# Kernel optimization log

Hardware: AMD Instinct MI355X
Metric: run time of the kernel (lower is better)

## Reference

```python
import jax, jax.numpy as jnp
import numpy as np

HEADS = 4
HID = 128
NEG_SLOPE = 0.2
N_NODES = 20000
N_EDGES = 320000
N_GRAPHS = 64
IN_DIM = 12


def gat_layer(x, src, dst, W, a_src, a_dst, b, n):
    # PyG GATConv, heads=4, concat=False (mean over heads), add_self_loops handled by caller.
    h = (x @ W).reshape(n, HEADS, HID)                      # [N,H,C]
    e_src = jnp.einsum('nhc,hc->nh', h, a_src)              # [N,H]
    e_dst = jnp.einsum('nhc,hc->nh', h, a_dst)
    e = jax.nn.leaky_relu(e_src[src] + e_dst[dst], NEG_SLOPE)  # [E,H]
    m = jax.lax.stop_gradient(jax.ops.segment_max(e, dst, num_segments=n))
    ex = jnp.exp(e - m[dst])
    denom = jax.ops.segment_sum(ex, dst, num_segments=n)    # [N,H]
    alpha = ex / denom[dst]                                 # edge softmax over incoming edges
    out = jax.ops.segment_sum(alpha[:, :, None] * h[src], dst, num_segments=n)  # [N,H,C]
    return out.mean(axis=1) + b                             # concat=False -> head mean, then bias


def setup_inputs() -> dict:
    key = jax.random.key(0)
    ks = jax.random.split(key, 20)
    def glorot(k, shape):
        lim = float(np.sqrt(6.0 / (shape[0] + shape[-1])))
        return jax.random.uniform(k, shape, jnp.float32, -lim, lim)
    inp = {
        'x': jax.random.normal(ks[0], (N_NODES, IN_DIM), jnp.float32),
        'edge_index': jax.random.randint(ks[1], (2, N_EDGES), 0, N_NODES, jnp.int64 if jax.config.jax_enable_x64 else jnp.int32),
        'batch': jnp.sort(jax.random.randint(ks[2], (N_NODES,), 0, N_GRAPHS)),
        'batch_size_tensor': jax.random.uniform(ks[3], (N_GRAPHS, 1), jnp.float32),
        # GAT layer 1
        'W1': glorot(ks[4], (IN_DIM, HEADS * HID)), 'as1': glorot(ks[5], (HEADS, HID)),
        'ad1': glorot(ks[6], (HEADS, HID)), 'b1': jnp.zeros((HID,), jnp.float32),
        # GAT layer 2
        'W2': glorot(ks[7], (HID, HEADS * HID)), 'as2': glorot(ks[8], (HEADS, HID)),
        'ad2': glorot(ks[9], (HEADS, HID)), 'b2': jnp.zeros((HID,), jnp.float32),
        # GAT layer 3
        'W3': glorot(ks[10], (HID, HEADS * HID)), 'as3': glorot(ks[11], (HEADS, HID)),
        'ad3': glorot(ks[12], (HEADS, HID)), 'b3': jnp.zeros((HID,), jnp.float32),
        # MLP: (128+1)->128->64->2
        'M1': glorot(ks[13], (HID + 1, HID)), 'mb1': jnp.zeros((HID,), jnp.float32),
        'M2': glorot(ks[14], (HID, HID // 2)), 'mb2': jnp.zeros((HID // 2,), jnp.float32),
        'M3': glorot(ks[15], (HID // 2, 2)), 'mb3': jnp.zeros((2,), jnp.float32),
    }
    return inp


def reference(x, edge_index, batch, batch_size_tensor,
              W1, as1, ad1, b1, W2, as2, ad2, b2, W3, as3, ad3, b3,
              M1, mb1, M2, mb2, M3, mb3):
    n = x.shape[0]
    loops = jnp.arange(n, dtype=edge_index.dtype)
    src = jnp.concatenate([edge_index[0], loops])   # add_self_loops=True (PyG default)
    dst = jnp.concatenate([edge_index[1], loops])
    h = jax.nn.relu(gat_layer(x, src, dst, W1, as1, ad1, b1, n))
    h = jax.nn.relu(gat_layer(h, src, dst, W2, as2, ad2, b2, n))
    h = jax.nn.relu(gat_layer(h, src, dst, W3, as3, ad3, b3, n))
    # global mean pool over graphs
    g = batch_size_tensor.shape[0]
    sums = jax.ops.segment_sum(h, batch, num_segments=g)
    cnts = jax.ops.segment_sum(jnp.ones((n,), h.dtype), batch, num_segments=g)
    pooled = sums / jnp.maximum(cnts, 1.0)[:, None]          # [G,128]
    bs = jnp.log1p(batch_size_tensor)                        # [G,1]
    z = jnp.concatenate([pooled, bs], axis=1)                # [G,129]
    z = jax.nn.relu(z @ M1 + mb1)                            # dropout(0.2) is identity at eval
    z = jax.nn.relu(z @ M2 + mb2)
    return z @ M3 + mb3                                      # [G,2]
```

## Files before the change

### kernel.cpp

```cpp
#include <hip/hip_runtime.h>
#include <hip/hip_bf16.h>
#include <math.h>

#define NN 20000
#define NE 320000
#define ET (NE + NN)
#define NG 64
#define HEADS 4
#define HID 128
#define OUTC (HEADS * HID)
#define SLOPE 0.2f

__device__ __forceinline__ float lrelu(float v) { return v > 0.f ? v : SLOPE * v; }

__global__ void k_hist(const int* __restrict__ ei, int* __restrict__ deg) {
  int e = blockIdx.x * blockDim.x + threadIdx.x;
  if (e >= ET) return;
  int dst = (e < NE) ? ei[NE + e] : (e - NE);
  atomicAdd(&deg[dst], 1);
}

__global__ void k_scan(const int* __restrict__ deg, int* __restrict__ row_start,
                       int* __restrict__ cursor) {
  __shared__ int sums[1024];
  int tid = threadIdx.x;
  const int PER = (NN + 1023) / 1024;
  int base = tid * PER;
  int local = 0;
  for (int i = 0; i < PER; ++i) { int idx = base + i; if (idx < NN) local += deg[idx]; }
  sums[tid] = local;
  __syncthreads();
  for (int off = 1; off < 1024; off <<= 1) {
    int v = (tid >= off) ? sums[tid - off] : 0;
    __syncthreads();
    sums[tid] += v;
    __syncthreads();
  }
  int run = sums[tid] - local;
  for (int i = 0; i < PER; ++i) {
    int idx = base + i;
    if (idx < NN) { row_start[idx] = run; cursor[idx] = run; run += deg[idx]; }
  }
  if (tid == 1023) row_start[NN] = sums[1023];
}

__global__ void k_scatter(const int* __restrict__ ei, int* __restrict__ cursor,
                          int* __restrict__ csr_src) {
  int e = blockIdx.x * blockDim.x + threadIdx.x;
  if (e >= ET) return;
  int src, dst;
  if (e < NE) { src = ei[e]; dst = ei[NE + e]; }
  else        { src = e - NE; dst = src; }
  int pos = atomicAdd(&cursor[dst], 1);
  csr_src[pos] = src;
}

__global__ void k_watt3(const float* __restrict__ W1, const float* __restrict__ as1,
                        const float* __restrict__ ad1, const float* __restrict__ W2,
                        const float* __restrict__ as2, const float* __restrict__ ad2,
                        const float* __restrict__ W3, const float* __restrict__ as3,
                        const float* __restrict__ ad3, float* __restrict__ watt1,
                        float* __restrict__ watt2, float* __restrict__ watt3) {
  int b = blockIdx.x;
  const float *W, *as, *ad;
  float* wo;
  int k;
  if (b < 12)       { k = b;       W = W1; as = as1; ad = ad1; wo = watt1; }
  else if (b < 140) { k = b - 12;  W = W2; as = as2; ad = ad2; wo = watt2; }
  else              { k = b - 140; W = W3; as = as3; ad = ad3; wo = watt3; }
  int tid = threadIdx.x;
  int t = tid & 7, h = t & 3;
  int c0 = (tid >> 3) * 4;
  const float* av = (t < 4 ? as : ad) + h * HID;
  const float* wr = W + (size_t)k * OUTC + h * HID;
  float4 wv = *reinterpret_cast<const float4*>(&wr[c0]);
  float4 a4 = *reinterpret_cast<const float4*>(&av[c0]);
  float p = wv.x * a4.x + wv.y * a4.y + wv.z * a4.z + wv.w * a4.w;
  __shared__ float lp[32][8];
  lp[tid >> 3][t] = p;
  __syncthreads();
  if (tid < 8) {
    float s = 0.f;
    for (int cc = 0; cc < 32; ++cc) s += lp[cc][tid];
    wo[k * 8 + tid] = s;
  }
}

__global__ void k_esd1(const float* __restrict__ x, const float* __restrict__ watt,
                       float* __restrict__ es, float* __restrict__ ed) {
  int n = blockIdx.x * blockDim.x + threadIdx.x;
  if (n >= NN) return;
  float xr[12];
#pragma unroll
  for (int k = 0; k < 12; ++k) xr[k] = x[(size_t)n * 12 + k];
#pragma unroll
  for (int t = 0; t < 8; ++t) {
    float acc = 0.f;
#pragma unroll
    for (int k = 0; k < 12; ++k) acc += xr[k] * watt[k * 8 + t];
    if (t < 4) es[n * 4 + t] = acc;
    else       ed[n * 4 + (t - 4)] = acc;
  }
}

__global__ void __launch_bounds__(256) k_esd128(
    const float* __restrict__ x, const float* __restrict__ watt,
    float* __restrict__ es, float* __restrict__ ed) {
  __shared__ float sw[HID * 8];
  int tid = threadIdx.x;
  for (int i = tid; i < HID * 8; i += 256) sw[i] = watt[i];
  __syncthreads();
  int wid = tid >> 6, lane = tid & 63;
  int gw = blockIdx.x * 4 + wid;
  int nw = gridDim.x * 4;
  for (int n = gw; n < NN; n += nw) {
    float2 xv = *reinterpret_cast<const float2*>(&x[(size_t)n * HID + lane * 2]);
    float p[8];
#pragma unroll
    for (int t = 0; t < 8; ++t)
      p[t] = xv.x * sw[(lane * 2) * 8 + t] + xv.y * sw[(lane * 2 + 1) * 8 + t];
#pragma unroll
    for (int t = 0; t < 8; ++t) {
#pragma unroll
      for (int off = 1; off < 64; off <<= 1) p[t] += __shfl_xor(p[t], off);
    }
    if (lane == 0) {
      es[n * 4 + 0] = p[0]; es[n * 4 + 1] = p[1];
      es[n * 4 + 2] = p[2]; es[n * 4 + 3] = p[3];
      ed[n * 4 + 0] = p[4]; ed[n * 4 + 1] = p[5];
      ed[n * 4 + 2] = p[6]; ed[n * 4 + 3] = p[7];
    }
  }
}

__global__ void __launch_bounds__(256) k_prep(
    const float* __restrict__ es, const float* __restrict__ ed,
    const int* __restrict__ row_start, const int* __restrict__ csr_src,
    float* __restrict__ ealpha, float* __restrict__ invd) {
  int wid = threadIdx.x >> 6;
  int lane = threadIdx.x & 63;
  int n = blockIdx.x * 4 + wid;
  int start = row_start[n];
  int deg = row_start[n + 1] - start;
  float4 edv = *reinterpret_cast<const float4*>(&ed[(size_t)n * 4]);
  float d0 = 0.f, d1 = 0.f, d2 = 0.f, d3 = 0.f;
  for (int k = lane; k < deg; k += 64) {
    int s = csr_src[start + k];
    float4 e4 = *reinterpret_cast<const float4*>(&es[(size_t)s * 4]);
    float4 ex;
    ex.x = __expf(lrelu(e4.x + edv.x));
    ex.y = __expf(lrelu(e4.y + edv.y));
    ex.z = __expf(lrelu(e4.z + edv.z));
    ex.w = __expf(lrelu(e4.w + edv.w));
    *reinterpret_cast<float4*>(&ealpha[(size_t)(start + k) * 4]) = ex;
    d0 += ex.x; d1 += ex.y; d2 += ex.z; d3 += ex.w;
  }
#pragma unroll
  for (int off = 1; off < 64; off <<= 1) {
    d0 += __shfl_xor(d0, off);
    d1 += __shfl_xor(d1, off);
    d2 += __shfl_xor(d2, off);
    d3 += __shfl_xor(d3, off);
  }
  if (lane == 0) {
    float4 iv;
    iv.x = 0.25f / d0; iv.y = 0.25f / d1; iv.z = 0.25f / d2; iv.w = 0.25f / d3;
    *reinterpret_cast<float4*>(&invd[(size_t)n * 4]) = iv;
  }
}

__global__ void __launch_bounds__(256, 4) k_aggx128(
    const float* __restrict__ x, const float* __restrict__ ealpha,
    const float* __restrict__ invd, const int* __restrict__ row_start,
    const int* __restrict__ csr_src, float* __restrict__ z) {
  int wid = threadIdx.x >> 6;
  int lane = threadIdx.x & 63;
  int n = blockIdx.x * 4 + wid;
  int start = row_start[n];
  int deg = row_start[n + 1] - start;
  const int* sp = csr_src + start;
  const float4* ap4 = reinterpret_cast<const float4*>(ealpha) + start;
  int c = lane * 2;
  float2 a0c = make_float2(0.f, 0.f), a1c = make_float2(0.f, 0.f);
  float2 a2c = make_float2(0.f, 0.f), a3c = make_float2(0.f, 0.f);
  int j = 0;
  for (; j + 4 <= deg; j += 4) {
    int s0 = sp[j + 0], s1 = sp[j + 1], s2 = sp[j + 2], s3 = sp[j + 3];
    float4 q0 = ap4[j + 0], q1 = ap4[j + 1], q2 = ap4[j + 2], q3 = ap4[j + 3];
    float2 x0 = *reinterpret_cast<const float2*>(&x[(size_t)s0 * HID + c]);
    float2 x1 = *reinterpret_cast<const float2*>(&x[(size_t)s1 * HID + c]);
    float2 x2 = *reinterpret_cast<const float2*>(&x[(size_t)s2 * HID + c]);
    float2 x3 = *reinterpret_cast<const float2*>(&x[(size_t)s3 * HID + c]);
    a0c.x += q0.x * x0.x; a0c.y += q0.x * x0.y;
    a1c.x += q0.y * x0.x; a1c.y += q0.y * x0.y;
    a2c.x += q0.z * x0.x; a2c.y += q0.z * x0.y;
    a3c.x += q0.w * x0.x; a3c.y += q0.w * x0.y;
    a0c.x += q1.x * x1.x; a0c.y += q1.x * x1.y;
    a1c.x += q1.y * x1.x; a1c.y += q1.y * x1.y;
    a2c.x += q1.z * x1.x; a2c.y += q1.z * x1.y;
    a3c.x += q1.w * x1.x; a3c.y += q1.w * x1.y;
    a0c.x += q2.x * x2.x; a0c.y += q2.x * x2.y;
    a1c.x += q2.y * x2.x; a1c.y += q2.y * x2.y;
    a2c.x += q2.z * x2.x; a2c.y += q2.z * x2.y;
    a3c.x += q2.w * x2.x; a3c.y += q2.w * x2.y;
    a0c.x += q3.x * x3.x; a0c.y += q3.x * x3.y;
    a1c.x += q3.y * x3.x; a1c.y += q3.y * x3.y;
    a2c.x += q3.z * x3.x; a2c.y += q3.z * x3.y;
    a3c.x += q3.w * x3.x; a3c.y += q3.w * x3.y;
  }
  for (; j < deg; ++j) {
    int s = sp[j];
    float4 q = ap4[j];
    float2 xv = *reinterpret_cast<const float2*>(&x[(size_t)s * HID + c]);
    a0c.x += q.x * xv.x; a0c.y += q.x * xv.y;
    a1c.x += q.y * xv.x; a1c.y += q.y * xv.y;
    a2c.x += q.z * xv.x; a2c.y += q.z * xv.y;
    a3c.x += q.w * xv.x; a3c.y += q.w * xv.y;
  }
  float4 iv = *reinterpret_cast<const float4*>(&invd[(size_t)n * 4]);
  a0c.x *= iv.x; a0c.y *= iv.x;
  a1c.x *= iv.y; a1c.y *= iv.y;
  a2c.x *= iv.z; a2c.y *= iv.z;
  a3c.x *= iv.w; a3c.y *= iv.w;
  float* zr = z + (size_t)n * OUTC;
  *reinterpret_cast<float2*>(&zr[0 * HID + c]) = a0c;
  *reinterpret_cast<float2*>(&zr[1 * HID + c]) = a1c;
  *reinterpret_cast<float2*>(&zr[2 * HID + c]) = a2c;
  *reinterpret_cast<float2*>(&zr[3 * HID + c]) = a3c;
}

__global__ void __launch_bounds__(256, 4) k_aggx1(
    const float* __restrict__ x, const float* __restrict__ ealpha,
    const float* __restrict__ invd, const int* __restrict__ row_start,
    const int* __restrict__ csr_src, float* __restrict__ z1) {
  int wid = threadIdx.x >> 6;
  int lane = threadIdx.x & 63;
  int n = blockIdx.x * 4 + wid;
  int start = row_start[n];
  int deg = row_start[n + 1] - start;
  const int* sp = csr_src + start;
  const float4* ap4 = reinterpret_cast<const float4*>(ealpha) + start;
  int h = lane >> 4;
  int cr = lane & 15;
  int cc = cr < 12 ? cr : 11;
  float acc = 0.f;
  int j = 0;
  for (; j + 4 <= deg; j += 4) {
    int s0 = sp[j + 0], s1 = sp[j + 1], s2 = sp[j + 2], s3 = sp[j + 3];
    float4 q0 = ap4[j + 0], q1 = ap4[j + 1], q2 = ap4[j + 2], q3 = ap4[j + 3];
    float ah0 = (h == 0) ? q0.x : (h == 1) ? q0.y : (h == 2) ? q0.z : q0.w;
    float ah1 = (h == 0) ? q1.x : (h == 1) ? q1.y : (h == 2) ? q1.z : q1.w;
    float ah2 = (h == 0) ? q2.x : (h == 1) ? q2.y : (h == 2) ? q2.z : q2.w;
    float ah3 = (h == 0) ? q3.x : (h == 1) ? q3.y : (h == 2) ? q3.z : q3.w;
    float x0 = x[(size_t)s0 * 12 + cc];
    float x1 = x[(size_t)s1 * 12 + cc];
    float x2 = x[(size_t)s2 * 12 + cc];
    float x3 = x[(size_t)s3 * 12 + cc];
    acc += ah0 * x0 + ah1 * x1 + ah2 * x2 + ah3 * x3;
  }
  for (; j < deg; ++j) {
    int s = sp[j];
    float4 q = ap4[j];
    float ah = (h == 0) ? q.x : (h == 1) ? q.y : (h == 2) ? q.z : q.w;
    acc += ah * x[(size_t)s * 12 + cc];
  }
  float ivh = invd[(size_t)n * 4 + h];
  if (cr < 12) z1[(size_t)n * 48 + h * 12 + cr] = acc * ivh;
}

template <int KTOT, int KH, int BK>
__global__ void k_gemm_full(const float* __restrict__ z, const float* __restrict__ W,
                            const float* __restrict__ bias, float* __restrict__ xout) {
  const int BM = 64, BN = 64;
  __shared__ float sAT[BK][BM + 4];
  __shared__ float sB[BK][BN];
  int tid = threadIdx.x;
  int r0 = blockIdx.y * BM;
  int cb = blockIdx.x * BN;
  int tx = tid & 15, ty = tid >> 4;
  int m0 = ty * 4, n0 = tx * 4;
  float acc[4][4] = {};
  for (int k0 = 0; k0 < KTOT; k0 += BK) {
    const int AF4 = BM * BK / 4;
    for (int idx = tid; idx < AF4; idx += 256) {
      int r = idx / (BK / 4);
      int kq = idx % (BK / 4);
      int row = r0 + r;
      float4 v = make_float4(0.f, 0.f, 0.f, 0.f);
      if (row < NN) v = *reinterpret_cast<const float4*>(&z[(size_t)row * KTOT + k0 + kq * 4]);
      sAT[kq * 4 + 0][r] = v.x;
      sAT[kq * 4 + 1][r] = v.y;
      sAT[kq * 4 + 2][r] = v.z;
      sAT[kq * 4 + 3][r] = v.w;
    }
    const int BF4 = BK * BN / 4;
    for (int idx = tid; idx < BF4; idx += 256) {
      int kr = idx / 16, nq = idx & 15;
      int kk = k0 + kr;
      int h = kk / KH, k = kk % KH;
      float4 v = *reinterpret_cast<const float4*>(&W[(size_t)k * OUTC + h * HID + cb + nq * 4]);
      *reinterpret_cast<float4*>(&sB[kr][nq * 4]) = v;
    }
    __syncthreads();
#pragma unroll 4
    for (int kk = 0; kk < BK; ++kk) {
      float4 a = *reinterpret_cast<const float4*>(&sAT[kk][m0]);
      float4 b = *reinterpret_cast<const float4*>(&sB[kk][n0]);
      acc[0][0] += a.x * b.x; acc[0][1] += a.x * b.y; acc[0][2] += a.x * b.z; acc[0][3] += a.x * b.w;
      acc[1][0] += a.y * b.x; acc[1][1] += a.y * b.y; acc[1][2] += a.y * b.z; acc[1][3] += a.y * b.w;
      acc[2][0] += a.z * b.x; acc[2][1] += a.z * b.y; acc[2][2] += a.z * b.z; acc[2][3] += a.z * b.w;
      acc[3][0] += a.w * b.x; acc[3][1] += a.w * b.y; acc[3][2] += a.w * b.z; acc[3][3] += a.w * b.w;
    }
    __syncthreads();
  }
  float4 bv = *reinterpret_cast<const float4*>(&bias[cb + n0]);
#pragma unroll
  for (int i = 0; i < 4; ++i) {
    int row = r0 + m0 + i;
    if (row < NN) {
      float4 o;
      o.x = fmaxf(acc[i][0] + bv.x, 0.f);
      o.y = fmaxf(acc[i][1] + bv.y, 0.f);
      o.z = fmaxf(acc[i][2] + bv.z, 0.f);
      o.w = fmaxf(acc[i][3] + bv.w, 0.f);
      *reinterpret_cast<float4*>(&xout[(size_t)row * HID + cb + n0]) = o;
    }
  }
}

template <int KTOT, int KH, int BK, int KCH>
__global__ void k_gemm_ks(const float* __restrict__ z, const float* __restrict__ W,
                          float* __restrict__ part) {
  const int BM = 64, BN = 64;
  __shared__ float sAT[BK][BM + 4];
  __shared__ float sB[BK][BN];
  int tid = threadIdx.x;
  int r0 = blockIdx.y * BM;
  int cb = blockIdx.x * BN;
  int kc = blockIdx.z;
  int tx = tid & 15, ty = tid >> 4;
  int m0 = ty * 4, n0 = tx * 4;
  float acc[4][4] = {};
  for (int k0 = kc * KCH; k0 < (kc + 1) * KCH; k0 += BK) {
    const int AF4 = BM * BK / 4;
    for (int idx = tid; idx < AF4; idx += 256) {
      int r = idx / (BK / 4);
      int kq = idx % (BK / 4);
      int row = r0 + r;
      float4 v = make_float4(0.f, 0.f, 0.f, 0.f);
      if (row < NN) v = *reinterpret_cast<const float4*>(&z[(size_t)row * KTOT + k0 + kq * 4]);
      sAT[kq * 4 + 0][r] = v.x;
      sAT[kq * 4 + 1][r] = v.y;
      sAT[kq * 4 + 2][r] = v.z;
      sAT[kq * 4 + 3][r] = v.w;
    }
    const int BF4 = BK * BN / 4;
    for (int idx = tid; idx < BF4; idx += 256) {
      int kr = idx / 16, nq = idx & 15;
      int kk = k0 + kr;
      int h = kk / KH, k = kk % KH;
      float4 v = *reinterpret_cast<const float4*>(&W[(size_t)k * OUTC + h * HID + cb + nq * 4]);
      *reinterpret_cast<float4*>(&sB[kr][nq * 4]) = v;
    }
    __syncthreads();
#pragma unroll 4
    for (int kk = 0; kk < BK; ++kk) {
      float4 a = *reinterpret_cast<const float4*>(&sAT[kk][m0]);
      float4 b = *reinterpret_cast<const float4*>(&sB[kk][n0]);
      acc[0][0] += a.x * b.x; acc[0][1] += a.x * b.y; acc[0][2] += a.x * b.z; acc[0][3] += a.x * b.w;
      acc[1][0] += a.y * b.x; acc[1][1] += a.y * b.y; acc[1][2] += a.y * b.z; acc[1][3] += a.y * b.w;
      acc[2][0] += a.z * b.x; acc[2][1] += a.z * b.y; acc[2][2] += a.z * b.z; acc[2][3] += a.z * b.w;
      acc[3][0] += a.w * b.x; acc[3][1] += a.w * b.y; acc[3][2] += a.w * b.z; acc[3][3] += a.w * b.w;
    }
    __syncthreads();
  }
#pragma unroll
  for (int i = 0; i < 4; ++i) {
    int row = r0 + m0 + i;
    if (row < NN) {
      float4 v = make_float4(acc[i][0], acc[i][1], acc[i][2], acc[i][3]);
      *reinterpret_cast<float4*>(&part[((size_t)kc * NN + row) * HID + cb + n0]) = v;
    }
  }
}

template <int POOL, int NKC>
__global__ void k_epi(const float* __restrict__ part, const float* __restrict__ bias,
                      const int* __restrict__ batch, float* __restrict__ xout,
                      float* __restrict__ gsums) {
  int tid = threadIdx.x;
  int row = blockIdx.x * 2 + (tid >> 7);
  int c = tid & 127;
  float o = bias[c];
#pragma unroll
  for (int kc = 0; kc < NKC; ++kc)
    o += part[((size_t)kc * NN + row) * HID + c];
  o = fmaxf(o, 0.f);
  if (POOL) {
    atomicAdd(&gsums[(size_t)batch[row] * HID + c], o);
  } else {
    xout[(size_t)row * HID + c] = o;
  }
}

__global__ void k_mlp(const float* __restrict__ sums, const int* __restrict__ batch,
                      const float* __restrict__ bst, const float* __restrict__ M1,
                      const float* __restrict__ mb1, const float* __restrict__ M2,
                      const float* __restrict__ mb2, const float* __restrict__ M3,
                      const float* __restrict__ mb3, float* __restrict__ out) {
  int g = blockIdx.x, tid = threadIdx.x;
  int lo = 0, hi = NN;
  while (lo < hi) { int mid = (lo + hi) >> 1; if (batch[mid] < g) lo = mid + 1; else hi = mid; }
  int s = lo;
  lo = s; hi = NN;
  while (lo < hi) { int mid = (lo + hi) >> 1; if (batch[mid] < g + 1) lo = mid + 1; else hi = mid; }
  int e = lo;
  float cnt = (float)(e - s);
  float pooled = sums[g * HID + tid] / fmaxf(cnt, 1.f);
  __shared__ float z[HID + 1];
  __shared__ float z1[HID];
  __shared__ float z2[64];
  z[tid] = pooled;
  if (tid == 0) z[HID] = log1pf(bst[g]);
  __syncthreads();
  float a1 = mb1[tid];
  for (int k = 0; k < HID + 1; ++k) a1 += z[k] * M1[k * HID + tid];
  z1[tid] = a1 > 0.f ? a1 : 0.f;
  __syncthreads();
  if (tid < 64) {
    float a2 = mb2[tid];
    for (int k = 0; k < HID; ++k) a2 += z1[k] * M2[k * 64 + tid];
    z2[tid] = a2 > 0.f ? a2 : 0.f;
  }
  __syncthreads();
  if (tid < 2) {
    float a3 = mb3[tid];
    for (int k = 0; k < 64; ++k) a3 += z2[k] * M3[k * 2 + tid];
    out[g * 2 + tid] = a3;
  }
}

extern "C" void kernel_launch(void* const* d_in, const int* in_sizes, int n_in,
                              void* d_out, int out_size, void* d_ws, size_t ws_size,
                              hipStream_t stream) {
  const float* x   = (const float*)d_in[0];
  const int*   ei  = (const int*)d_in[1];
  const int*   bat = (const int*)d_in[2];
  const float* bst = (const float*)d_in[3];
  const float* W1 = (const float*)d_in[4];
  const float* as1 = (const float*)d_in[5];
  const float* ad1 = (const float*)d_in[6];
  const float* b1 = (const float*)d_in[7];
  const float* W2 = (const float*)d_in[8];
  const float* as2 = (const float*)d_in[9];
  const float* ad2 = (const float*)d_in[10];
  const float* b2 = (const float*)d_in[11];
  const float* W3 = (const float*)d_in[12];
  const float* as3 = (const float*)d_in[13];
  const float* ad3 = (const float*)d_in[14];
  const float* b3 = (const float*)d_in[15];
  const float* M1 = (const float*)d_in[16];
  const float* mb1 = (const float*)d_in[17];
  const float* M2 = (const float*)d_in[18];
  const float* mb2 = (const float*)d_in[19];
  const float* M3 = (const float*)d_in[20];
  const float* mb3 = (const float*)d_in[21];
  float* out = (float*)d_out;

  const bool use4 = ws_size >= (size_t)110 * 1024 * 1024;

  char* ws = (char*)d_ws;
  auto alloc = [&](size_t bytes) -> void* {
    void* p = (void*)ws;
    ws += (bytes + 255) & ~(size_t)255;
    return p;
  };
  float* z_buf  = (float*)alloc((size_t)NN * OUTC * 4);
  float* z1_buf = (float*)alloc((size_t)NN * 48 * 4);
  float* x_buf  = (float*)alloc((size_t)NN * HID * 4);
  float* e_src  = (float*)alloc((size_t)NN * 4 * 4);
  float* e_dst  = (float*)alloc((size_t)NN * 4 * 4);
  int*   deg    = (int*)alloc((size_t)NN * 4);
  int*   rowst  = (int*)alloc((size_t)(NN + 1) * 4);
  int*   cursor = (int*)alloc((size_t)NN * 4);
  int*   csr    = (int*)alloc((size_t)ET * 4);
  float* ealpha = (float*)alloc((size_t)ET * 4 * 4);
  float* part   = (float*)alloc((size_t)(use4 ? 4 : 2) * NN * HID * 4);
  float* invd   = (float*)alloc((size_t)NN * 4 * 4);
  float* watt1  = (float*)alloc((size_t)12 * 8 * 4);
  float* watt2  = (float*)alloc((size_t)HID * 8 * 4);
  float* watt3  = (float*)alloc((size_t)HID * 8 * 4);
  float* gsums  = (float*)alloc((size_t)NG * HID * 4);

  hipMemsetAsync(deg, 0, (size_t)NN * 4, stream);
  hipMemsetAsync(gsums, 0, (size_t)NG * HID * 4, stream);
  k_hist<<<(ET + 255) / 256, 256, 0, stream>>>(ei, deg);
  k_scan<<<1, 1024, 0, stream>>>(deg, rowst, cursor);
  k_scatter<<<(ET + 255) / 256, 256, 0, stream>>>(ei, cursor, csr);
  k_watt3<<<268, 256, 0, stream>>>(W1, as1, ad1, W2, as2, ad2, W3, as3, ad3,
                                   watt1, watt2, watt3);

  dim3 pgrid(NN / 4);
  dim3 g1grid(2, (NN + 63) / 64);
  dim3 ks4grid(2, (NN + 63) / 64, 4);
  dim3 ks2grid(2, (NN + 63) / 64, 2);
  dim3 epigrid(NN / 2);
  k_esd1<<<(NN + 255) / 256, 256, 0, stream>>>(x, watt1, e_src, e_dst);
  k_prep<<<pgrid, 256, 0, stream>>>(e_src, e_dst, rowst, csr, ealpha, invd);
  k_aggx1<<<pgrid, 256, 0, stream>>>(x, ealpha, invd, rowst, csr, z1_buf);
  k_gemm_full<48, 12, 48><<<g1grid, 256, 0, stream>>>(z1_buf, W1, b1, x_buf);
  k_esd128<<<512, 256, 0, stream>>>(x_buf, watt2, e_src, e_dst);
  k_prep<<<pgrid, 256, 0, stream>>>(e_src, e_dst, rowst, csr, ealpha, invd);
  k_aggx128<<<pgrid, 256, 0, stream>>>(x_buf, ealpha, invd, rowst, csr, z_buf);
  if (use4) {
    k_gemm_ks<512, 128, 64, 128><<<ks4grid, 256, 0, stream>>>(z_buf, W2, part);
    k_epi<0, 4><<<epigrid, 256, 0, stream>>>(part, b2, bat, x_buf, gsums);
  } else {
    k_gemm_ks<512, 128, 64, 256><<<ks2grid, 256, 0, stream>>>(z_buf, W2, part);
    k_epi<0, 2><<<epigrid, 256, 0, stream>>>(part, b2, bat, x_buf, gsums);
  }
  k_esd128<<<512, 256, 0, stream>>>(x_buf, watt3, e_src, e_dst);
  k_prep<<<pgrid, 256, 0, stream>>>(e_src, e_dst, rowst, csr, ealpha, invd);
  k_aggx128<<<pgrid, 256, 0, stream>>>(x_buf, ealpha, invd, rowst, csr, z_buf);
  if (use4) {
    k_gemm_ks<512, 128, 64, 128><<<ks4grid, 256, 0, stream>>>(z_buf, W3, part);
    k_epi<1, 4><<<epigrid, 256, 0, stream>>>(part, b3, bat, x_buf, gsums);
  } else {
    k_gemm_ks<512, 128, 64, 256><<<ks2grid, 256, 0, stream>>>(z_buf, W3, part);
    k_epi<1, 2><<<epigrid, 256, 0, stream>>>(part, b3, bat, x_buf, gsums);
  }
  k_mlp<<<NG, 128, 0, stream>>>(gsums, bat, bst, M1, mb1, M2, mb2, M3, mb3, out);
}
```

Before: 378.9 us.

## Fuse edge-softmax prep into aggregation kernels via per-wave LDS staging

```diff
diff --git a/kernel.cpp b/kernel.cpp
--- a/kernel.cpp
+++ b/kernel.cpp
@@ -133,95 +133,90 @@
   }
 }
 
-__global__ void __launch_bounds__(256) k_prep(
-    const float* __restrict__ es, const float* __restrict__ ed,
-    const int* __restrict__ row_start, const int* __restrict__ csr_src,
-    float* __restrict__ ealpha, float* __restrict__ invd) {
-  int wid = threadIdx.x >> 6;
-  int lane = threadIdx.x & 63;
-  int n = blockIdx.x * 4 + wid;
-  int start = row_start[n];
-  int deg = row_start[n + 1] - start;
-  float4 edv = *reinterpret_cast<const float4*>(&ed[(size_t)n * 4]);
-  float d0 = 0.f, d1 = 0.f, d2 = 0.f, d3 = 0.f;
-  for (int k = lane; k < deg; k += 64) {
-    int s = csr_src[start + k];
-    float4 e4 = *reinterpret_cast<const float4*>(&es[(size_t)s * 4]);
-    float4 ex;
-    ex.x = __expf(lrelu(e4.x + edv.x));
-    ex.y = __expf(lrelu(e4.y + edv.y));
-    ex.z = __expf(lrelu(e4.z + edv.z));
-    ex.w = __expf(lrelu(e4.w + edv.w));
-    *reinterpret_cast<float4*>(&ealpha[(size_t)(start + k) * 4]) = ex;
-    d0 += ex.x; d1 += ex.y; d2 += ex.z; d3 += ex.w;
-  }
-#pragma unroll
-  for (int off = 1; off < 64; off <<= 1) {
-    d0 += __shfl_xor(d0, off);
-    d1 += __shfl_xor(d1, off);
-    d2 += __shfl_xor(d2, off);
-    d3 += __shfl_xor(d3, off);
-  }
-  if (lane == 0) {
-    float4 iv;
-    iv.x = 0.25f / d0; iv.y = 0.25f / d1; iv.z = 0.25f / d2; iv.w = 0.25f / d3;
-    *reinterpret_cast<float4*>(&invd[(size_t)n * 4]) = iv;
-  }
-}
-
-__global__ void __launch_bounds__(256, 4) k_aggx128(
-    const float* __restrict__ x, const float* __restrict__ ealpha,
-    const float* __restrict__ invd, const int* __restrict__ row_start,
+__global__ void __launch_bounds__(256, 4) k_aggf(
+    const float* __restrict__ x, const float* __restrict__ es,
+    const float* __restrict__ ed, const int* __restrict__ row_start,
     const int* __restrict__ csr_src, float* __restrict__ z) {
+  __shared__ float sal[4][256];
   int wid = threadIdx.x >> 6;
   int lane = threadIdx.x & 63;
   int n = blockIdx.x * 4 + wid;
   int start = row_start[n];
   int deg = row_start[n + 1] - start;
   const int* sp = csr_src + start;
-  const float4* ap4 = reinterpret_cast<const float4*>(ealpha) + start;
+  float4 edv = *reinterpret_cast<const float4*>(&ed[(size_t)n * 4]);
   int c = lane * 2;
   float2 a0c = make_float2(0.f, 0.f), a1c = make_float2(0.f, 0.f);
   float2 a2c = make_float2(0.f, 0.f), a3c = make_float2(0.f, 0.f);
-  int j = 0;
-  for (; j + 4 <= deg; j += 4) {
-    int s0 = sp[j + 0], s1 = sp[j + 1], s2 = sp[j + 2], s3 = sp[j + 3];
-    float4 q0 = ap4[j + 0], q1 = ap4[j + 1], q2 = ap4[j + 2], q3 = ap4[j + 3];
-    float2 x0 = *reinterpret_cast<const float2*>(&x[(size_t)s0 * HID + c]);
-    float2 x1 = *reinterpret_cast<const float2*>(&x[(size_t)s1 * HID + c]);
-    float2 x2 = *reinterpret_cast<const float2*>(&x[(size_t)s2 * HID + c]);
-    float2 x3 = *reinterpret_cast<const float2*>(&x[(size_t)s3 * HID + c]);
-    a0c.x += q0.x * x0.x; a0c.y += q0.x * x0.y;
-    a1c.x += q0.y * x0.x; a1c.y += q0.y * x0.y;
-    a2c.x += q0.z * x0.x; a2c.y += q0.z * x0.y;
-    a3c.x += q0.w * x0.x; a3c.y += q0.w * x0.y;
-    a0c.x += q1.x * x1.x; a0c.y += q1.x * x1.y;
-    a1c.x += q1.y * x1.x; a1c.y += q1.y * x1.y;
-    a2c.x += q1.z * x1.x; a2c.y += q1.z * x1.y;
-    a3c.x += q1.w * x1.x; a3c.y += q1.w * x1.y;
-    a0c.x += q2.x * x2.x; a0c.y += q2.x * x2.y;
-    a1c.x += q2.y * x2.x; a1c.y += q2.y * x2.y;
-    a2c.x += q2.z * x2.x; a2c.y += q2.z * x2.y;
-    a3c.x += q2.w * x2.x; a3c.y += q2.w * x2.y;
-    a0c.x += q3.x * x3.x; a0c.y += q3.x * x3.y;
-    a1c.x += q3.y * x3.x; a1c.y += q3.y * x3.y;
-    a2c.x += q3.z * x3.x; a2c.y += q3.z * x3.y;
-    a3c.x += q3.w * x3.x; a3c.y += q3.w * x3.y;
-  }
-  for (; j < deg; ++j) {
-    int s = sp[j];
-    float4 q = ap4[j];
-    float2 xv = *reinterpret_cast<const float2*>(&x[(size_t)s * HID + c]);
-    a0c.x += q.x * xv.x; a0c.y += q.x * xv.y;
-    a1c.x += q.y * xv.x; a1c.y += q.y * xv.y;
-    a2c.x += q.z * xv.x; a2c.y += q.z * xv.y;
-    a3c.x += q.w * xv.x; a3c.y += q.w * xv.y;
-  }
-  float4 iv = *reinterpret_cast<const float4*>(&invd[(size_t)n * 4]);
-  a0c.x *= iv.x; a0c.y *= iv.x;
-  a1c.x *= iv.y; a1c.y *= iv.y;
-  a2c.x *= iv.z; a2c.y *= iv.z;
-  a3c.x *= iv.w; a3c.y *= iv.w;
+  float d0 = 0.f, d1 = 0.f, d2 = 0.f, d3 = 0.f;
+  for (int cb = 0; cb < deg; cb += 64) {
+    int m = min(64, deg - cb);
+    {
+      int kk = cb + ((lane < m) ? lane : (m - 1));
+      int s = sp[kk];
+      float4 e4 = *reinterpret_cast<const float4*>(&es[(size_t)s * 4]);
+      float4 ex;
+      ex.x = __expf(lrelu(e4.x + edv.x));
+      ex.y = __expf(lrelu(e4.y + edv.y));
+      ex.z = __expf(lrelu(e4.z + edv.z));
+      ex.w = __expf(lrelu(e4.w + edv.w));
+      if (lane < m) {
+        *reinterpret_cast<float4*>(&sal[wid][lane * 4]) = ex;
+        d0 += ex.x; d1 += ex.y; d2 += ex.z; d3 += ex.w;
+      }
+    }
+    asm volatile("s_waitcnt lgkmcnt(0)" ::: "memory");
+    int j = 0;
+    for (; j + 4 <= m; j += 4) {
+      float4 q0 = *reinterpret_cast<const float4*>(&sal[wid][(j + 0) * 4]);
+      float4 q1 = *reinterpret_cast<const float4*>(&sal[wid][(j + 1) * 4]);
+      float4 q2 = *reinterpret_cast<const float4*>(&sal[wid][(j + 2) * 4]);
+      float4 q3 = *reinterpret_cast<const float4*>(&sal[wid][(j + 3) * 4]);
+      int s0 = sp[cb + j + 0], s1 = sp[cb + j + 1];
+      int s2 = sp[cb + j + 2], s3 = sp[cb + j + 3];
+      float2 x0 = *reinterpret_cast<const float2*>(&x[(size_t)s0 * HID + c]);
+      float2 x1 = *reinterpret_cast<const float2*>(&x[(size_t)s1 * HID + c]);
+      float2 x2 = *reinterpret_cast<const float2*>(&x[(size_t)s2 * HID + c]);
+      float2 x3 = *reinterpret_cast<const float2*>(&x[(size_t)s3 * HID + c]);
+      a0c.x += q0.x * x0.x; a0c.y += q0.x * x0.y;
+      a1c.x += q0.y * x0.x; a1c.y += q0.y * x0.y;
+      a2c.x += q0.z * x0.x; a2c.y += q0.z * x0.y;
+      a3c.x += q0.w * x0.x; a3c.y += q0.w * x0.y;
+      a0c.x += q1.x * x1.x; a0c.y += q1.x * x1.y;
+      a1c.x += q1.y * x1.x; a1c.y += q1.y * x1.y;
+      a2c.x += q1.z * x1.x; a2c.y += q1.z * x1.y;
+      a3c.x += q1.w * x1.x; a3c.y += q1.w * x1.y;
+      a0c.x += q2.x * x2.x; a0c.y += q2.x * x2.y;
+      a1c.x += q2.y * x2.x; a1c.y += q2.y * x2.y;
+      a2c.x += q2.z * x2.x; a2c.y += q2.z * x2.y;
+      a3c.x += q2.w * x2.x; a3c.y += q2.w * x2.y;
+      a0c.x += q3.x * x3.x; a0c.y += q3.x * x3.y;
+      a1c.x += q3.y * x3.x; a1c.y += q3.y * x3.y;
+      a2c.x += q3.z * x3.x; a2c.y += q3.z * x3.y;
+      a3c.x += q3.w * x3.x; a3c.y += q3.w * x3.y;
+    }
+    for (; j < m; ++j) {
+      float4 q = *reinterpret_cast<const float4*>(&sal[wid][j * 4]);
+      int s = sp[cb + j];
+      float2 xv = *reinterpret_cast<const float2*>(&x[(size_t)s * HID + c]);
+      a0c.x += q.x * xv.x; a0c.y += q.x * xv.y;
+      a1c.x += q.y * xv.x; a1c.y += q.y * xv.y;
+      a2c.x += q.z * xv.x; a2c.y += q.z * xv.y;
+      a3c.x += q.w * xv.x; a3c.y += q.w * xv.y;
+    }
+  }
+#pragma unroll
+  for (int off = 1; off < 64; off <<= 1) {
+    d0 += __shfl_xor(d0, off);
+    d1 += __shfl_xor(d1, off);
+    d2 += __shfl_xor(d2, off);
+    d3 += __shfl_xor(d3, off);
+  }
+  float i0 = 0.25f / d0, i1 = 0.25f / d1, i2 = 0.25f / d2, i3 = 0.25f / d3;
+  a0c.x *= i0; a0c.y *= i0;
+  a1c.x *= i1; a1c.y *= i1;
+  a2c.x *= i2; a2c.y *= i2;
+  a3c.x *= i3; a3c.y *= i3;
   float* zr = z + (size_t)n * OUTC;
   *reinterpret_cast<float2*>(&zr[0 * HID + c]) = a0c;
   *reinterpret_cast<float2*>(&zr[1 * HID + c]) = a1c;
@@ -229,42 +224,69 @@
   *reinterpret_cast<float2*>(&zr[3 * HID + c]) = a3c;
 }
 
-__global__ void __launch_bounds__(256, 4) k_aggx1(
-    const float* __restrict__ x, const float* __restrict__ ealpha,
-    const float* __restrict__ invd, const int* __restrict__ row_start,
+__global__ void __launch_bounds__(256, 4) k_aggf1(
+    const float* __restrict__ x, const float* __restrict__ es,
+    const float* __restrict__ ed, const int* __restrict__ row_start,
     const int* __restrict__ csr_src, float* __restrict__ z1) {
+  __shared__ float sal[4][256];
   int wid = threadIdx.x >> 6;
   int lane = threadIdx.x & 63;
   int n = blockIdx.x * 4 + wid;
   int start = row_start[n];
   int deg = row_start[n + 1] - start;
   const int* sp = csr_src + start;
-  const float4* ap4 = reinterpret_cast<const float4*>(ealpha) + start;
+  float4 edv = *reinterpret_cast<const float4*>(&ed[(size_t)n * 4]);
   int h = lane >> 4;
   int cr = lane & 15;
   int cc = cr < 12 ? cr : 11;
   float acc = 0.f;
-  int j = 0;
-  for (; j + 4 <= deg; j += 4) {
-    int s0 = sp[j + 0], s1 = sp[j + 1], s2 = sp[j + 2], s3 = sp[j + 3];
-    float4 q0 = ap4[j + 0], q1 = ap4[j + 1], q2 = ap4[j + 2], q3 = ap4[j + 3];
-    float ah0 = (h == 0) ? q0.x : (h == 1) ? q0.y : (h == 2) ? q0.z : q0.w;
-    float ah1 = (h == 0) ? q1.x : (h == 1) ? q1.y : (h == 2) ? q1.z : q1.w;
-    float ah2 = (h == 0) ? q2.x : (h == 1) ? q2.y : (h == 2) ? q2.z : q2.w;
-    float ah3 = (h == 0) ? q3.x : (h == 1) ? q3.y : (h == 2) ? q3.z : q3.w;
-    float x0 = x[(size_t)s0 * 12 + cc];
-    float x1 = x[(size_t)s1 * 12 + cc];
-    float x2 = x[(size_t)s2 * 12 + cc];
-    float x3 = x[(size_t)s3 * 12 + cc];
-    acc += ah0 * x0 + ah1 * x1 + ah2 * x2 + ah3 * x3;
-  }
-  for (; j < deg; ++j) {
-    int s = sp[j];
-    float4 q = ap4[j];
-    float ah = (h == 0) ? q.x : (h == 1) ? q.y : (h == 2) ? q.z : q.w;
-    acc += ah * x[(size_t)s * 12 + cc];
-  }
-  float ivh = invd[(size_t)n * 4 + h];
+  float d0 = 0.f, d1 = 0.f, d2 = 0.f, d3 = 0.f;
+  for (int cb = 0; cb < deg; cb += 64) {
+    int m = min(64, deg - cb);
+    {
+      int kk = cb + ((lane < m) ? lane : (m - 1));
+      int s = sp[kk];
+      float4 e4 = *reinterpret_cast<const float4*>(&es[(size_t)s * 4]);
+      float4 ex;
+      ex.x = __expf(lrelu(e4.x + edv.x));
+      ex.y = __expf(lrelu(e4.y + edv.y));
+      ex.z = __expf(lrelu(e4.z + edv.z));
+      ex.w = __expf(lrelu(e4.w + edv.w));
+      if (lane < m) {
+        *reinterpret_cast<float4*>(&sal[wid][lane * 4]) = ex;
+        d0 += ex.x; d1 += ex.y; d2 += ex.z; d3 += ex.w;
+      }
+    }
+    asm volatile("s_waitcnt lgkmcnt(0)" ::: "memory");
+    int j = 0;
+    for (; j + 4 <= m; j += 4) {
+      float ah0 = sal[wid][(j + 0) * 4 + h];
+      float ah1 = sal[wid][(j + 1) * 4 + h];
+      float ah2 = sal[wid][(j + 2) * 4 + h];
+      float ah3 = sal[wid][(j + 3) * 4 + h];
+      int s0 = sp[cb + j + 0], s1 = sp[cb + j + 1];
+      int s2 = sp[cb + j + 2], s3 = sp[cb + j + 3];
+      float x0 = x[(size_t)s0 * 12 + cc];
+      float x1 = x[(size_t)s1 * 12 + cc];
+      float x2 = x[(size_t)s2 * 12 + cc];
+      float x3 = x[(size_t)s3 * 12 + cc];
+      acc += ah0 * x0 + ah1 * x1 + ah2 * x2 + ah3 * x3;
+    }
+    for (; j < m; ++j) {
+      float ah = sal[wid][j * 4 + h];
+      int s = sp[cb + j];
+      acc += ah * x[(size_t)s * 12 + cc];
+    }
+  }
+#pragma unroll
+  for (int off = 1; off < 64; off <<= 1) {
+    d0 += __shfl_xor(d0, off);
+    d1 += __shfl_xor(d1, off);
+    d2 += __shfl_xor(d2, off);
+    d3 += __shfl_xor(d3, off);
+  }
+  float dh = (h == 0) ? d0 : (h == 1) ? d1 : (h == 2) ? d2 : d3;
+  float ivh = 0.25f / dh;
   if (cr < 12) z1[(size_t)n * 48 + h * 12 + cr] = acc * ivh;
 }
 
@@ -484,9 +506,7 @@
   int*   rowst  = (int*)alloc((size_t)(NN + 1) * 4);
   int*   cursor = (int*)alloc((size_t)NN * 4);
   int*   csr    = (int*)alloc((size_t)ET * 4);
-  float* ealpha = (float*)alloc((size_t)ET * 4 * 4);
   float* part   = (float*)alloc((size_t)(use4 ? 4 : 2) * NN * HID * 4);
-  float* invd   = (float*)alloc((size_t)NN * 4 * 4);
   float* watt1  = (float*)alloc((size_t)12 * 8 * 4);
   float* watt2  = (float*)alloc((size_t)HID * 8 * 4);
   float* watt3  = (float*)alloc((size_t)HID * 8 * 4);
@@ -506,27 +526,24 @@
   dim3 ks2grid(2, (NN + 63) / 64, 2);
   dim3 epigrid(NN / 2);
   k_esd1<<<(NN + 255) / 256, 256, 0, stream>>>(x, watt1, e_src, e_dst);
-  k_prep<<<pgrid, 256, 0, stream>>>(e_src, e_dst, rowst, csr, ealpha, invd);
-  k_aggx1<<<pgrid, 256, 0, stream>>>(x, ealpha, invd, rowst, csr, z1_buf);
+  k_aggf1<<<pgrid, 256, 0, stream>>>(x, e_src, e_dst, rowst, csr, z1_buf);
   k_gemm_full<48, 12, 48><<<g1grid, 256, 0, stream>>>(z1_buf, W1, b1, x_buf);
   k_esd128<<<512, 256, 0, stream>>>(x_buf, watt2, e_src, e_dst);
-  k_prep<<<pgrid, 256, 0, stream>>>(e_src, e_dst, rowst, csr, ealpha, invd);
-  k_aggx128<<<pgrid, 256, 0, stream>>>(x_buf, ealpha, invd, rowst, csr, z_buf);
+  k_aggf<<<pgrid, 256, 0, stream>>>(x_buf, e_src, e_dst, rowst, csr, z_buf);
   if (use4) {
-    k_gemm_ks<512, 128, 64, 128><<<ks4grid, 256, 0, stream>>>(z_buf, W2, part);
+    k_gemm_ks<512, 128, 32, 128><<<ks4grid, 256, 0, stream>>>(z_buf, W2, part);
     k_epi<0, 4><<<epigrid, 256, 0, stream>>>(part, b2, bat, x_buf, gsums);
   } else {
-    k_gemm_ks<512, 128, 64, 256><<<ks2grid, 256, 0, stream>>>(z_buf, W2, part);
+    k_gemm_ks<512, 128, 32, 256><<<ks2grid, 256, 0, stream>>>(z_buf, W2, part);
     k_epi<0, 2><<<epigrid, 256, 0, stream>>>(part, b2, bat, x_buf, gsums);
   }
   k_esd128<<<512, 256, 0, stream>>>(x_buf, watt3, e_src, e_dst);
-  k_prep<<<pgrid, 256, 0, stream>>>(e_src, e_dst, rowst, csr, ealpha, invd);
-  k_aggx128<<<pgrid, 256, 0, stream>>>(x_buf, ealpha, invd, rowst, csr, z_buf);
+  k_aggf<<<pgrid, 256, 0, stream>>>(x_buf, e_src, e_dst, rowst, csr, z_buf);
   if (use4) {
-    k_gemm_ks<512, 128, 64, 128><<<ks4grid, 256, 0, stream>>>(z_buf, W3, part);
+    k_gemm_ks<512, 128, 32, 128><<<ks4grid, 256, 0, stream>>>(z_buf, W3, part);
     k_epi<1, 4><<<epigrid, 256, 0, stream>>>(part, b3, bat, x_buf, gsums);
   } else {
-    k_gemm_ks<512, 128, 64, 256><<<ks2grid, 256, 0, stream>>>(z_buf, W3, part);
+    k_gemm_ks<512, 128, 32, 256><<<ks2grid, 256, 0, stream>>>(z_buf, W3, part);
     k_epi<1, 2><<<epigrid, 256, 0, stream>>>(part, b3, bat, x_buf, gsums);
   }
   k_mlp<<<NG, 128, 0, stream>>>(gsums, bat, bst, M1, mb1, M2, mb2, M3, mb3, out);
```

Result: faster. 345.5 us (-8.8%).
